# Kernel optimization log

Hardware: AMD Instinct MI355X
Metric: run time of the kernel (lower is better)

## Reference

```python
import jax, jax.numpy as jnp
import numpy as np

V, D, H, L, E = 50000, 128, 128, 4, 160000


def setup_inputs() -> dict:
    key = jax.random.key(0)
    ks = jax.random.split(key, 8)
    inp = {
        "node_embeddings": jax.random.normal(ks[0], (V, D), dtype=jnp.float32),
        "adj0": jax.random.randint(ks[1], (E, 2), 0, V, dtype=jnp.int32),
        "adj1": jax.random.randint(ks[2], (E, 2), 0, V, dtype=jnp.int32),
        "adj2": jax.random.randint(ks[3], (E, 2), 0, V, dtype=jnp.int32),
        "adj3": jax.random.randint(ks[4], (E, 2), 0, V, dtype=jnp.int32),
        # One MLP per (edge_type, endpoint): Linear(2D->H) -> relu -> Linear(H->H), no biases
        "W1": jax.random.normal(ks[5], (L, 2, 2 * D, H), dtype=jnp.float32) * 0.05,
        "W2": jax.random.normal(ks[6], (L, 2, H, H), dtype=jnp.float32) * 0.05,
    }
    return inp


def reference(node_embeddings, adj0, adj1, adj2, adj3, W1, W2):
    num_nodes = node_embeddings.shape[0]
    msgs = []
    tgts = []
    for l, adj in enumerate((adj0, adj1, adj2, adj3)):
        # gather both endpoint states and concat -> [E, 2D]
        src = node_embeddings[adj[:, 0]]
        dst = node_embeddings[adj[:, 1]]
        raw = jnp.concatenate([src, dst], axis=-1)
        # one MLP per endpoint; messages sent to that endpoint's node
        for ep in range(2):
            h = jax.nn.relu(raw @ W1[l, ep])          # [E, H]
            msgs.append(h @ W2[l, ep])                 # [E, H]
            tgts.append(adj[:, ep])
    messages = jnp.concatenate(msgs, axis=0)          # [L*2*E, H]
    targets = jnp.concatenate(tgts, axis=0)           # [L*2*E]
    agg = jax.ops.segment_sum(messages, targets, num_segments=num_nodes)  # [V, H]
    return jax.nn.relu(agg)
```

## Files before the change

### kernel.cpp

```cpp
#include <hip/hip_runtime.h>

#define V_NODES 50000
#define NEDGE   160000
#define NSEG    (8 * V_NODES)

typedef __bf16 bf16;
typedef __attribute__((ext_vector_type(8))) __bf16 bf16x8;
typedef __attribute__((ext_vector_type(4))) __bf16 bf16x4;
typedef __attribute__((ext_vector_type(4))) float  f32x4;

__device__ __forceinline__ int clampV(int n) {
  unsigned u = (unsigned)n;
  return (int)(u < (unsigned)V_NODES ? u : (unsigned)(V_NODES - 1));
}

__device__ __forceinline__ float bflo(unsigned u) {
  return __builtin_bit_cast(float, u << 16);
}
__device__ __forceinline__ float bfhi(unsigned u) {
  return __builtin_bit_cast(float, u & 0xffff0000u);
}


__global__ __launch_bounds__(256) void prep_emb_k(const float* __restrict__ in,
                                                  bf16* __restrict__ out) {
  int i = blockIdx.x * 256 + threadIdx.x;
  float4 v = ((const float4*)in)[i];
  bf16x4 o = {(bf16)v.x, (bf16)v.y, (bf16)v.z, (bf16)v.w};
  *(bf16x4*)(out + (size_t)i * 4) = o;
}

__global__ __launch_bounds__(256) void prep_w1_k(const float* __restrict__ in,
                                                 bf16* __restrict__ out) {
  int idx = blockIdx.x * 256 + threadIdx.x;
  int n = idx & 127, k = (idx >> 7) & 255, g = idx >> 15;
  out[(((g << 7) + n) << 8) + k] = (bf16)in[idx];
}

__global__ __launch_bounds__(256) void prep_w2_k(const float* __restrict__ in,
                                                 bf16* __restrict__ out) {
  int idx = blockIdx.x * 256 + threadIdx.x;
  int n = idx & 127, k = (idx >> 7) & 127, g = idx >> 14;
  out[(((g << 7) + n) << 7) + k] = (bf16)in[idx];
}

__global__ __launch_bounds__(256) void relu_k(float* __restrict__ out) {
  int i = blockIdx.x * 256 + threadIdx.x;
  float4 v = ((float4*)out)[i];
  v.x = fmaxf(v.x, 0.f); v.y = fmaxf(v.y, 0.f);
  v.z = fmaxf(v.z, 0.f); v.w = fmaxf(v.w, 0.f);
  ((float4*)out)[i] = v;
}


__global__ __launch_bounds__(256) void fused_prep_k(
    const float* __restrict__ emb, const float* __restrict__ W1,
    const float* __restrict__ W2,
    const int* __restrict__ a0, const int* __restrict__ a1,
    const int* __restrict__ a2, const int* __restrict__ a3,
    bf16* __restrict__ embB, bf16* __restrict__ w1t, bf16* __restrict__ w2t,
    int* __restrict__ counts) {
  const int bx = blockIdx.x, tid = threadIdx.x;
  if (bx < 6250) {
    int i = bx * 256 + tid;
    float4 v = ((const float4*)emb)[i];
    bf16x4 o = {(bf16)v.x, (bf16)v.y, (bf16)v.z, (bf16)v.w};
    *(bf16x4*)(embB + (size_t)i * 4) = o;
  } else if (bx < 7274) {
    int idx = (bx - 6250) * 256 + tid;
    int n = idx & 127, k = (idx >> 7) & 255, g = idx >> 15;
    w1t[(((g << 7) + n) << 8) + k] = (bf16)W1[idx];
  } else if (bx < 7786) {
    int idx = (bx - 7274) * 256 + tid;
    int n = idx & 127, k = (idx >> 7) & 127, g = idx >> 14;
    w2t[(((g << 7) + n) << 7) + k] = (bf16)W2[idx];
  } else {
    int j = bx - 7786;
    int g = j / 625;
    int e = (j - g * 625) * 256 + tid;
    int l = g >> 1, ep = g & 1;
    const int* adj = (l == 0) ? a0 : (l == 1) ? a1 : (l == 2) ? a2 : a3;
    int tgt = clampV(adj[2 * e + ep]);
    atomicAdd(&counts[g * V_NODES + tgt], 1);
  }
}


__global__ __launch_bounds__(256) void scan_a_k(const int* __restrict__ counts,
                                                int* __restrict__ offs1,
                                                int* __restrict__ bsums) {
  __shared__ int sh[256];
  int t = threadIdx.x, base = blockIdx.x * 512;
  int e0 = base + 2 * t, e1 = e0 + 1;
  int a = (e0 < NSEG) ? counts[e0] : 0;
  int b = (e1 < NSEG) ? counts[e1] : 0;
  int s = a + b;
  sh[t] = s;
  __syncthreads();
  #pragma unroll
  for (int d = 1; d < 256; d <<= 1) {
    int v = (t >= d) ? sh[t - d] : 0;
    __syncthreads();
    sh[t] += v;
    __syncthreads();
  }
  int excl = sh[t] - s;
  if (e0 < NSEG) offs1[e0] = excl;
  if (e1 < NSEG) offs1[e1] = excl + a;
  if (t == 255) bsums[blockIdx.x] = sh[255];
}

#define NBLK_SCAN 782

__global__ __launch_bounds__(256) void scan_b_k(int* __restrict__ bsums,
                                                int* __restrict__ offsX) {
  __shared__ int sh[NBLK_SCAN];
  int t = threadIdx.x;
  for (int i = t; i < NBLK_SCAN; i += 256) sh[i] = bsums[i];
  __syncthreads();
  if (t == 0) {
    int run = 0;
    for (int i = 0; i < NBLK_SCAN; ++i) { int v = sh[i]; sh[i] = run; run += v; }
    offsX[0] = 0;
  }
  __syncthreads();
  for (int i = t; i < NBLK_SCAN; i += 256) bsums[i] = sh[i];
}

__global__ __launch_bounds__(256) void scan_c_k(int* __restrict__ offs1,
                                                const int* __restrict__ bsums) {
  int i = blockIdx.x * 256 + threadIdx.x;
  if (i < NSEG) offs1[i] += bsums[i >> 9];
}


__global__ __launch_bounds__(256) void fused_xg_sc_k(
    const bf16* __restrict__ embB, const bf16* __restrict__ w1t,
    bf16* __restrict__ Xab,
    const int* __restrict__ a0, const int* __restrict__ a1,
    const int* __restrict__ a2, const int* __restrict__ a3,
    int* __restrict__ offs1, int* __restrict__ ids,
    int gbase, int nxg) {
  const int tid = threadIdx.x;
  if ((int)blockIdx.x < nxg) {
    const int slot = blockIdx.x / 625;
    const int bxx  = blockIdx.x - slot * 625;
    const int w = tid >> 6, lane = tid & 63;
    const int l15 = lane & 15, q = lane >> 4;
    const int h2 = w >> 1, dh = w & 1;
    const int g = gbase + slot;

    bf16x8 wA[4][4];
    const bf16* __restrict__ w1g = w1t + (size_t)g * 32768;
    #pragma unroll
    for (int mb = 0; mb < 4; ++mb)
      #pragma unroll
      for (int kb = 0; kb < 4; ++kb)
        wA[mb][kb] = *(const bf16x8*)(w1g + (size_t)(dh * 64 + mb * 16 + l15) * 256 +
                                      h2 * 128 + kb * 32 + q * 8);

    bf16* __restrict__ Xh = Xab + (size_t)slot * 12800000 + (size_t)h2 * 6400000;

    #pragma unroll
    for (int t = 0; t < 5; ++t) {
      const int node = bxx * 80 + t * 16 + l15;
      bf16x8 b[4];
      #pragma unroll
      for (int kb = 0; kb < 4; ++kb)
        b[kb] = *(const bf16x8*)(embB + (size_t)node * 128 + kb * 32 + q * 8);

      f32x4 acc[4] = {};
      #pragma unroll
      for (int kb = 0; kb < 4; ++kb)
        #pragma unroll
        for (int mb = 0; mb < 4; ++mb)
          acc[mb] = __builtin_amdgcn_mfma_f32_16x16x32_bf16(wA[mb][kb], b[kb], acc[mb], 0, 0, 0);

      bf16* basep = Xh + (size_t)node * 128 + dh * 64 + q * 4;
      #pragma unroll
      for (int mb = 0; mb < 4; ++mb) {
        bf16x4 o = {(bf16)acc[mb][0], (bf16)acc[mb][1],
                    (bf16)acc[mb][2], (bf16)acc[mb][3]};
        *(bf16x4*)(basep + mb * 16) = o;
      }
    }
  } else {
    int j = blockIdx.x - nxg;
    int g = j / 625;
    int e = (j - g * 625) * 256 + tid;
    int l = g >> 1, ep = g & 1;
    const int* adj = (l == 0) ? a0 : (l == 1) ? a1 : (l == 2) ? a2 : a3;
    int2 pr = ((const int2*)adj)[e];
    int src = clampV(pr.x), dst = clampV(pr.y);
    int tgt = ep ? dst : src;
    int oth = ep ? src : dst;
    int pos = atomicAdd(&offs1[g * V_NODES + tgt], 1);
    ids[pos] = oth;
  }
}


__global__ __launch_bounds__(256) void aggf4_k(
    const bf16* __restrict__ Xab,
    const int* __restrict__ offsX, const int* __restrict__ ids,
    bf16* __restrict__ HaggB, int gbase) {
  const int wv = threadIdx.x >> 6, lane = threadIdx.x & 63;
  const int h = lane >> 5, m = lane & 31;
  const int node = blockIdx.x * 8 + wv * 2 + h;
  const int slot = blockIdx.y, g = gbase + slot;
  const int ep = g & 1;
  const bf16* __restrict__ Xa = Xab + (size_t)slot * 12800000;
  const bf16* __restrict__ Xb = Xa + 6400000;
  const bf16* __restrict__ own = ep ? Xb : Xa;
  const bf16* __restrict__ oth = ep ? Xa : Xb;
  const int seg = g * V_NODES + node;
  const int beg = offsX[seg], end = offsX[seg + 1];

  uint2 uo = *(const uint2*)(own + (size_t)node * 128 + m * 4);
  const float o0 = bflo(uo.x), o1 = bfhi(uo.x);
  const float o2 = bflo(uo.y), o3 = bfhi(uo.y);

  float s0 = 0.f, s1 = 0.f, s2 = 0.f, s3 = 0.f;
  int i = beg;
  for (; i + 2 <= end; i += 2) {
    int n0 = ids[i];
    int n1 = ids[i + 1];
    uint2 u0 = *(const uint2*)(oth + (size_t)n0 * 128 + m * 4);
    uint2 u1 = *(const uint2*)(oth + (size_t)n1 * 128 + m * 4);
    s0 += fmaxf(o0 + bflo(u0.x), 0.f) + fmaxf(o0 + bflo(u1.x), 0.f);
    s1 += fmaxf(o1 + bfhi(u0.x), 0.f) + fmaxf(o1 + bfhi(u1.x), 0.f);
    s2 += fmaxf(o2 + bflo(u0.y), 0.f) + fmaxf(o2 + bflo(u1.y), 0.f);
    s3 += fmaxf(o3 + bfhi(u0.y), 0.f) + fmaxf(o3 + bfhi(u1.y), 0.f);
  }
  if (i < end) {
    int n = ids[i];
    uint2 u = *(const uint2*)(oth + (size_t)n * 128 + m * 4);
    s0 += fmaxf(o0 + bflo(u.x), 0.f);
    s1 += fmaxf(o1 + bfhi(u.x), 0.f);
    s2 += fmaxf(o2 + bflo(u.y), 0.f);
    s3 += fmaxf(o3 + bfhi(u.y), 0.f);
  }
  bf16x4 st = {(bf16)s0, (bf16)s1, (bf16)s2, (bf16)s3};
  *(bf16x4*)(HaggB + ((size_t)g * V_NODES + node) * 128 + m * 4) = st;
}


__global__ __launch_bounds__(256) void gemm2p_k(const bf16* __restrict__ HaggB,
                                                const bf16* __restrict__ w2t,
                                                float* __restrict__ out) {
  __shared__ __attribute__((aligned(16))) bf16 a_lds[32 * 128];

  const int tid = threadIdx.x, wv = tid >> 6, lane = tid & 63;
  const int l15 = lane & 15, q = lane >> 4;
  const int v0 = blockIdx.x * 32;

  const int srow = tid >> 3, sc0 = (tid & 7) * 2;
  bf16* sp0 = &a_lds[srow * 128 + ((sc0 ^ (srow & 7)) << 3)];
  bf16* sp1 = &a_lds[srow * 128 + (((sc0 + 1) ^ (srow & 7)) << 3)];

  const uint4* Hg = (const uint4*)(HaggB + (size_t)v0 * 128);
  uint4 s0 = Hg[tid * 2], s1 = Hg[tid * 2 + 1];

  f32x4 acc[2][2] = {};
  for (int g = 0; g < 8; ++g) {
    __syncthreads();
    *(uint4*)sp0 = s0;
    *(uint4*)sp1 = s1;
    if (g < 7) {
      const uint4* Hn = (const uint4*)(HaggB + (size_t)(g + 1) * 6400000 +
                                       (size_t)v0 * 128);
      s0 = Hn[tid * 2];
      s1 = Hn[tid * 2 + 1];
    }
    __syncthreads();

    const bf16* __restrict__ Wb = w2t + (size_t)g * 16384;
    #pragma unroll
    for (int kb = 0; kb < 4; ++kb) {
      bf16x8 a[2];
      #pragma unroll
      for (int mt = 0; mt < 2; ++mt) {
        int r = mt * 16 + l15;
        a[mt] = *(const bf16x8*)(&a_lds[r * 128 + (((kb * 4 + q) ^ (r & 7)) << 3)]);
      }
      #pragma unroll
      for (int t = 0; t < 2; ++t) {
        int n = (wv * 2 + t) * 16 + l15;
        bf16x8 b = *(const bf16x8*)(Wb + (size_t)n * 128 + kb * 32 + q * 8);
        #pragma unroll
        for (int mt = 0; mt < 2; ++mt)
          acc[mt][t] = __builtin_amdgcn_mfma_f32_16x16x32_bf16(a[mt], b, acc[mt][t], 0, 0, 0);
      }
    }
  }

  #pragma unroll
  for (int mt = 0; mt < 2; ++mt)
    #pragma unroll
    for (int r = 0; r < 4; ++r) {
      int row = v0 + mt * 16 + q * 4 + r;
      if (row < V_NODES) {
        #pragma unroll
        for (int t = 0; t < 2; ++t) {
          int col = (wv * 2 + t) * 16 + l15;
          out[(size_t)row * 128 + col] = fmaxf(acc[mt][t][r], 0.f);
        }
      }
    }
}


__global__ __launch_bounds__(256) void edge_k(
    const bf16* __restrict__ embB,
    const int* __restrict__ a0, const int* __restrict__ a1,
    const int* __restrict__ a2, const int* __restrict__ a3,
    const bf16* __restrict__ w1t, const bf16* __restrict__ w2t,
    float* __restrict__ out) {

  __shared__ __attribute__((aligned(16))) bf16 w1_lds[128 * 256];
  __shared__ __attribute__((aligned(16))) bf16 h_lds[64 * 128];

  const int tid = threadIdx.x;
  const int g  = blockIdx.x >> 6;
  const int bs = blockIdx.x & 63;
  const int l = g >> 1, ep = g & 1;
  const int* __restrict__ adj = (l == 0) ? a0 : (l == 1) ? a1 : (l == 2) ? a2 : a3;

  {
    const uint4* w1g = (const uint4*)(w1t + (size_t)g * 128 * 256);
    #pragma unroll
    for (int i = 0; i < 16; ++i) {
      int j = i * 256 + tid;
      int n = j >> 5, c = j & 31;
      *(uint4*)(&w1_lds[n * 256 + ((c ^ (n & 7)) << 3)]) = w1g[j];
    }
  }
  __syncthreads();

  const int w    = tid >> 6;
  const int lane = tid & 63;
  const int wr = w >> 1, wc = w & 1;
  const int l15 = lane & 15, q = lane >> 4;
  const bf16* __restrict__ w2g = w2t + (size_t)g * 128 * 128;

  for (int t = bs; t < 2500; t += 64) {
    const int ebase = t * 64;
    int2 pr0 = ((const int2*)adj)[ebase + 32 * wr + l15];
    int2 pr1 = ((const int2*)adj)[ebase + 32 * wr + 16 + l15];
    pr0.x = clampV(pr0.x); pr0.y = clampV(pr0.y);
    pr1.x = clampV(pr1.x); pr1.y = clampV(pr1.y);

    f32x4 acc[2][4] = {};
    #pragma unroll
    for (int kb = 0; kb < 8; ++kb) {
      const int k = kb * 32 + q * 8;
      const int klo = k & 127;
      const int n0 = (kb < 4) ? pr0.x : pr0.y;
      const int n1 = (kb < 4) ? pr1.x : pr1.y;
      bf16x8 a[2], b[4];
      a[0] = *(const bf16x8*)(embB + (size_t)n0 * 128 + klo);
      a[1] = *(const bf16x8*)(embB + (size_t)n1 * 128 + klo);
      const int csw = ((kb << 2) + q);
      #pragma unroll
      for (int nt = 0; nt < 4; ++nt) {
        int n = 64 * wc + 16 * nt + l15;
        b[nt] = *(const bf16x8*)(&w1_lds[n * 256 + ((csw ^ (l15 & 7)) << 3)]);
      }
      #pragma unroll
      for (int mt = 0; mt < 2; ++mt)
        #pragma unroll
        for (int nt = 0; nt < 4; ++nt)
          acc[mt][nt] = __builtin_amdgcn_mfma_f32_16x16x32_bf16(a[mt], b[nt], acc[mt][nt], 0, 0, 0);
    }

    __syncthreads();
    #pragma unroll
    for (int mt = 0; mt < 2; ++mt)
      #pragma unroll
      for (int nt = 0; nt < 4; ++nt)
        #pragma unroll
        for (int r = 0; r < 4; ++r) {
          float v = acc[mt][nt][r];
          v = v > 0.f ? v : 0.f;
          int row = 32 * wr + 16 * mt + 4 * q + r;
          int col = 64 * wc + 16 * nt + l15;
          int c = col >> 3;
          h_lds[row * 128 + (((c ^ (row & 7)) << 3) | (col & 7))] = (bf16)v;
        }
    __syncthreads();

    f32x4 acc2[2][4] = {};
    #pragma unroll
    for (int kb = 0; kb < 4; ++kb) {
      const int k = kb * 32 + q * 8;
      const int csw = (kb << 2) + q;
      bf16x8 a[2], b[4];
      #pragma unroll
      for (int mt = 0; mt < 2; ++mt) {
        int row = 32 * wr + 16 * mt + l15;
        a[mt] = *(const bf16x8*)(&h_lds[row * 128 + ((csw ^ (row & 7)) << 3)]);
      }
      #pragma unroll
      for (int nt = 0; nt < 4; ++nt) {
        int n = 64 * wc + 16 * nt + l15;
        b[nt] = *(const bf16x8*)(w2g + n * 128 + k);
      }
      #pragma unroll
      for (int mt = 0; mt < 2; ++mt)
        #pragma unroll
        for (int nt = 0; nt < 4; ++nt)
          acc2[mt][nt] = __builtin_amdgcn_mfma_f32_16x16x32_bf16(a[mt], b[nt], acc2[mt][nt], 0, 0, 0);
    }

    #pragma unroll
    for (int mt = 0; mt < 2; ++mt)
      #pragma unroll
      for (int r = 0; r < 4; ++r) {
        int row = 32 * wr + 16 * mt + 4 * q + r;
        int2 pr = ((const int2*)adj)[ebase + row];
        int node = clampV(ep ? pr.y : pr.x);
        float* basep = out + (size_t)node * 128 + 64 * wc + l15;
        #pragma unroll
        for (int nt = 0; nt < 4; ++nt)
          unsafeAtomicAdd(basep + 16 * nt, acc2[mt][nt][r]);
      }
  }
}


extern "C" void kernel_launch(void* const* d_in, const int* in_sizes, int n_in,
                              void* d_out, int out_size, void* d_ws, size_t ws_size,
                              hipStream_t stream) {
  const float* emb = (const float*)d_in[0];
  const int* a0 = (const int*)d_in[1];
  const int* a1 = (const int*)d_in[2];
  const int* a2 = (const int*)d_in[3];
  const int* a3 = (const int*)d_in[4];
  const float* W1 = (const float*)d_in[5];
  const float* W2 = (const float*)d_in[6];
  float* out = (float*)d_out;

  char* ws = (char*)d_ws;
  bf16* embB   = (bf16*)(ws);
  bf16* w1t    = (bf16*)(ws + 12800000);
  bf16* w2t    = (bf16*)(ws + 13324288);
  int*  offsX  = (int*) (ws + 13586432);
  int*  ids    = (int*) (ws + 15186448);
  int*  bsums  = (int*) (ws + 20306448);
  int*  counts = (int*) (ws + 20309584);
  bf16* HaggB  = (bf16*)(ws + 21909584);
  bf16* Xab    = (bf16*)(ws + 124309584);
  const size_t fixedsz = 124309584;
  int* offs1 = offsX + 1;

  int GG = 0;
  if      (ws_size >= fixedsz + 8ull * 25600000) GG = 8;
  else if (ws_size >= fixedsz + 4ull * 25600000) GG = 4;
  else if (ws_size >= fixedsz + 2ull * 25600000) GG = 2;
  else if (ws_size >= fixedsz + 1ull * 25600000) GG = 1;

  if (GG) {
    hipMemsetAsync(counts, 0, 1600000, stream);
    fused_prep_k<<<12786, 256, 0, stream>>>(emb, W1, W2, a0, a1, a2, a3,
                                            embB, w1t, w2t, counts);
    scan_a_k<<<NBLK_SCAN, 256, 0, stream>>>(counts, offs1, bsums);
    scan_b_k<<<1, 256, 0, stream>>>(bsums, offsX);
    scan_c_k<<<1563, 256, 0, stream>>>(offs1, bsums);

    fused_xg_sc_k<<<625 * GG + 5000, 256, 0, stream>>>(
        embB, w1t, Xab, a0, a1, a2, a3, offs1, ids, 0, 625 * GG);
    aggf4_k<<<dim3(6250, GG), 256, 0, stream>>>(Xab, offsX, ids, HaggB, 0);

    for (int gb = GG; gb < 8; gb += GG) {
      fused_xg_sc_k<<<625 * GG, 256, 0, stream>>>(
          embB, w1t, Xab, a0, a1, a2, a3, offs1, ids, gb, 625 * GG);
      aggf4_k<<<dim3(6250, GG), 256, 0, stream>>>(Xab, offsX, ids, HaggB, gb);
    }
    gemm2p_k<<<1563, 256, 0, stream>>>(HaggB, w2t, out);
  } else {
    prep_emb_k<<<6250, 256, 0, stream>>>(emb, embB);
    prep_w1_k<<<1024, 256, 0, stream>>>(W1, w1t);
    prep_w2_k<<<512, 256, 0, stream>>>(W2, w2t);
    hipMemsetAsync(d_out, 0, 25600000, stream);
    edge_k<<<512, 256, 0, stream>>>(embB, a0, a1, a2, a3, w1t, w2t, out);
    relu_k<<<6250, 256, 0, stream>>>(out);
  }
}
```

Baseline: 507.2 us.

## Fuse own-side projection, aggregation and second GEMM into one per-node kernel

The first-layer precompute now writes only the 'other endpoint' projection for each group, through an LDS-staged, coalesced store. The own-endpoint projection is recomputed per node inside a new fused kernel. That kernel also does the neighbor gather-relu-sum and the W2 matmul in LDS, accumulating across all 8 groups and applying the final relu. This removes the HaggB intermediate, the half of Xab that held the own side, and the separate gemm2 pass, which cuts global memory traffic and the number of launches. The cost is extra MFMA work for the own projection and serialized per-group barriers inside each block.

```diff
diff --git a/kernel.cpp b/kernel.cpp
--- a/kernel.cpp
+++ b/kernel.cpp
@@ -136,19 +136,20 @@
 
 __global__ __launch_bounds__(256) void fused_xg_sc_k(
     const bf16* __restrict__ embB, const bf16* __restrict__ w1t,
-    bf16* __restrict__ Xab,
+    bf16* __restrict__ Xg,
     const int* __restrict__ a0, const int* __restrict__ a1,
     const int* __restrict__ a2, const int* __restrict__ a3,
-    int* __restrict__ offs1, int* __restrict__ ids,
-    int gbase, int nxg) {
+    int* __restrict__ offs1, int* __restrict__ ids, int nxg) {
+  __shared__ __attribute__((aligned(16))) bf16 stg[2 * 16 * 128];
   const int tid = threadIdx.x;
+
   if ((int)blockIdx.x < nxg) {
-    const int slot = blockIdx.x / 625;
-    const int bxx  = blockIdx.x - slot * 625;
+    const int gp = blockIdx.x / 625, bxx = blockIdx.x - gp * 625;
     const int w = tid >> 6, lane = tid & 63;
     const int l15 = lane & 15, q = lane >> 4;
     const int h2 = w >> 1, dh = w & 1;
-    const int g = gbase + slot;
+    const int g = gp * 2 + h2;
+    const int goff = h2 ? 0 : 128;
 
     bf16x8 wA[4][4];
     const bf16* __restrict__ w1g = w1t + (size_t)g * 32768;
@@ -157,13 +158,15 @@
       #pragma unroll
       for (int kb = 0; kb < 4; ++kb)
         wA[mb][kb] = *(const bf16x8*)(w1g + (size_t)(dh * 64 + mb * 16 + l15) * 256 +
-                                      h2 * 128 + kb * 32 + q * 8);
-
-    bf16* __restrict__ Xh = Xab + (size_t)slot * 12800000 + (size_t)h2 * 6400000;
-
-    #pragma unroll
+                                      goff + kb * 32 + q * 8);
+
+    const int oh = tid >> 7, ln = tid & 127;
+    const int srow = ln >> 3, ch0 = (ln & 7) * 2;
+    const size_t gobase = (size_t)(gp * 2 + oh) * 6400000;
+
     for (int t = 0; t < 5; ++t) {
-      const int node = bxx * 80 + t * 16 + l15;
+      const int nodeB = bxx * 80 + t * 16;
+      const int node = nodeB + l15;
       bf16x8 b[4];
       #pragma unroll
       for (int kb = 0; kb < 4; ++kb)
@@ -176,12 +179,22 @@
         for (int mb = 0; mb < 4; ++mb)
           acc[mb] = __builtin_amdgcn_mfma_f32_16x16x32_bf16(wA[mb][kb], b[kb], acc[mb], 0, 0, 0);
 
-      bf16* basep = Xh + (size_t)node * 128 + dh * 64 + q * 4;
+      if (t) __syncthreads();
       #pragma unroll
       for (int mb = 0; mb < 4; ++mb) {
+        int d0 = dh * 64 + mb * 16 + q * 4;
+        int c = d0 >> 3, sub = (q & 1) * 8;
         bf16x4 o = {(bf16)acc[mb][0], (bf16)acc[mb][1],
                     (bf16)acc[mb][2], (bf16)acc[mb][3]};
-        *(bf16x4*)(basep + mb * 16) = o;
+        *(bf16x4*)((char*)stg + h2 * 4096 + l15 * 256 + ((c ^ (l15 & 7)) << 4) + sub) = o;
+      }
+      __syncthreads();
+      #pragma unroll
+      for (int cc = 0; cc < 2; ++cc) {
+        int ch = ch0 + cc;
+        uint4 v = *(const uint4*)((char*)stg + oh * 4096 + srow * 256 +
+                                  ((ch ^ (srow & 7)) << 4));
+        *(uint4*)(Xg + gobase + (size_t)(nodeB + srow) * 128 + ch * 8) = v;
       }
     }
   } else {
@@ -200,112 +213,112 @@
 }
 
 
-__global__ __launch_bounds__(256) void aggf4_k(
-    const bf16* __restrict__ Xab,
+__global__ __launch_bounds__(256) void agg2_k(
+    const bf16* __restrict__ embB, const bf16* __restrict__ w1t,
+    const bf16* __restrict__ w2t, const bf16* __restrict__ Xg,
     const int* __restrict__ offsX, const int* __restrict__ ids,
-    bf16* __restrict__ HaggB, int gbase) {
-  const int wv = threadIdx.x >> 6, lane = threadIdx.x & 63;
-  const int h = lane >> 5, m = lane & 31;
-  const int node = blockIdx.x * 8 + wv * 2 + h;
-  const int slot = blockIdx.y, g = gbase + slot;
-  const int ep = g & 1;
-  const bf16* __restrict__ Xa = Xab + (size_t)slot * 12800000;
-  const bf16* __restrict__ Xb = Xa + 6400000;
-  const bf16* __restrict__ own = ep ? Xb : Xa;
-  const bf16* __restrict__ oth = ep ? Xa : Xb;
-  const int seg = g * V_NODES + node;
-  const int beg = offsX[seg], end = offsX[seg + 1];
-
-  uint2 uo = *(const uint2*)(own + (size_t)node * 128 + m * 4);
-  const float o0 = bflo(uo.x), o1 = bfhi(uo.x);
-  const float o2 = bflo(uo.y), o3 = bfhi(uo.y);
-
-  float s0 = 0.f, s1 = 0.f, s2 = 0.f, s3 = 0.f;
-  int i = beg;
-  for (; i + 2 <= end; i += 2) {
-    int n0 = ids[i];
-    int n1 = ids[i + 1];
-    uint2 u0 = *(const uint2*)(oth + (size_t)n0 * 128 + m * 4);
-    uint2 u1 = *(const uint2*)(oth + (size_t)n1 * 128 + m * 4);
-    s0 += fmaxf(o0 + bflo(u0.x), 0.f) + fmaxf(o0 + bflo(u1.x), 0.f);
-    s1 += fmaxf(o1 + bfhi(u0.x), 0.f) + fmaxf(o1 + bfhi(u1.x), 0.f);
-    s2 += fmaxf(o2 + bflo(u0.y), 0.f) + fmaxf(o2 + bflo(u1.y), 0.f);
-    s3 += fmaxf(o3 + bfhi(u0.y), 0.f) + fmaxf(o3 + bfhi(u1.y), 0.f);
-  }
-  if (i < end) {
-    int n = ids[i];
-    uint2 u = *(const uint2*)(oth + (size_t)n * 128 + m * 4);
-    s0 += fmaxf(o0 + bflo(u.x), 0.f);
-    s1 += fmaxf(o1 + bfhi(u.x), 0.f);
-    s2 += fmaxf(o2 + bflo(u.y), 0.f);
-    s3 += fmaxf(o3 + bfhi(u.y), 0.f);
-  }
-  bf16x4 st = {(bf16)s0, (bf16)s1, (bf16)s2, (bf16)s3};
-  *(bf16x4*)(HaggB + ((size_t)g * V_NODES + node) * 128 + m * 4) = st;
-}
-
-
-__global__ __launch_bounds__(256) void gemm2p_k(const bf16* __restrict__ HaggB,
-                                                const bf16* __restrict__ w2t,
-                                                float* __restrict__ out) {
-  __shared__ __attribute__((aligned(16))) bf16 a_lds[32 * 128];
+    float* __restrict__ out) {
+  __shared__ __attribute__((aligned(16))) bf16 ownT[16 * 128];
+  __shared__ __attribute__((aligned(16))) bf16 Ht[16 * 128];
 
   const int tid = threadIdx.x, wv = tid >> 6, lane = tid & 63;
   const int l15 = lane & 15, q = lane >> 4;
-  const int v0 = blockIdx.x * 32;
-
-  const int srow = tid >> 3, sc0 = (tid & 7) * 2;
-  bf16* sp0 = &a_lds[srow * 128 + ((sc0 ^ (srow & 7)) << 3)];
-  bf16* sp1 = &a_lds[srow * 128 + (((sc0 + 1) ^ (srow & 7)) << 3)];
-
-  const uint4* Hg = (const uint4*)(HaggB + (size_t)v0 * 128);
-  uint4 s0 = Hg[tid * 2], s1 = Hg[tid * 2 + 1];
-
-  f32x4 acc[2][2] = {};
+  const int v0 = blockIdx.x * 16;
+  const int qw = tid >> 4, j = tid & 15;
+
+  bf16x8 be[4];
+  #pragma unroll
+  for (int kb = 0; kb < 4; ++kb)
+    be[kb] = *(const bf16x8*)(embB + (size_t)(v0 + l15) * 128 + kb * 32 + q * 8);
+
+  f32x4 aco[2] = {};
+
   for (int g = 0; g < 8; ++g) {
-    __syncthreads();
-    *(uint4*)sp0 = s0;
-    *(uint4*)sp1 = s1;
-    if (g < 7) {
-      const uint4* Hn = (const uint4*)(HaggB + (size_t)(g + 1) * 6400000 +
-                                       (size_t)v0 * 128);
-      s0 = Hn[tid * 2];
-      s1 = Hn[tid * 2 + 1];
-    }
-    __syncthreads();
-
-    const bf16* __restrict__ Wb = w2t + (size_t)g * 16384;
+    const int ownoff = (g & 1) ? 128 : 0;
+    const bf16* __restrict__ w1g = w1t + (size_t)g * 32768;
+
+    f32x4 oc[2] = {};
+    #pragma unroll
+    for (int kb = 0; kb < 4; ++kb)
+      #pragma unroll
+      for (int t = 0; t < 2; ++t) {
+        int m = (wv * 2 + t) * 16 + l15;
+        bf16x8 a = *(const bf16x8*)(w1g + (size_t)m * 256 + ownoff + kb * 32 + q * 8);
+        oc[t] = __builtin_amdgcn_mfma_f32_16x16x32_bf16(a, be[kb], oc[t], 0, 0, 0);
+      }
+    #pragma unroll
+    for (int t = 0; t < 2; ++t) {
+      int d0 = (wv * 2 + t) * 16 + q * 4;
+      int c = d0 >> 3, sub = (q & 1) * 8;
+      bf16x4 o = {(bf16)oc[t][0], (bf16)oc[t][1], (bf16)oc[t][2], (bf16)oc[t][3]};
+      *(bf16x4*)((char*)ownT + l15 * 256 + ((c ^ (l15 & 7)) << 4) + sub) = o;
+    }
+    __syncthreads();
+
+    {
+      const int nd = qw;
+      const int seg = g * V_NODES + v0 + nd;
+      const int beg = offsX[seg], end = offsX[seg + 1];
+      uint4 uo = *(const uint4*)((char*)ownT + nd * 256 + ((j ^ (nd & 7)) << 4));
+      const float o0 = bflo(uo.x), o1 = bfhi(uo.x), o2 = bflo(uo.y), o3 = bfhi(uo.y);
+      const float o4 = bflo(uo.z), o5 = bfhi(uo.z), o6 = bflo(uo.w), o7 = bfhi(uo.w);
+      const bf16* __restrict__ Xgg = Xg + (size_t)g * 6400000;
+
+      float s0 = 0.f, s1 = 0.f, s2 = 0.f, s3 = 0.f;
+      float s4 = 0.f, s5 = 0.f, s6 = 0.f, s7 = 0.f;
+      int i = beg;
+      for (; i + 2 <= end; i += 2) {
+        int n0 = ids[i], n1 = ids[i + 1];
+        uint4 u0 = *(const uint4*)(Xgg + (size_t)n0 * 128 + j * 8);
+        uint4 u1 = *(const uint4*)(Xgg + (size_t)n1 * 128 + j * 8);
+        s0 += fmaxf(o0 + bflo(u0.x), 0.f) + fmaxf(o0 + bflo(u1.x), 0.f);
+        s1 += fmaxf(o1 + bfhi(u0.x), 0.f) + fmaxf(o1 + bfhi(u1.x), 0.f);
+        s2 += fmaxf(o2 + bflo(u0.y), 0.f) + fmaxf(o2 + bflo(u1.y), 0.f);
+        s3 += fmaxf(o3 + bfhi(u0.y), 0.f) + fmaxf(o3 + bfhi(u1.y), 0.f);
+        s4 += fmaxf(o4 + bflo(u0.z), 0.f) + fmaxf(o4 + bflo(u1.z), 0.f);
+        s5 += fmaxf(o5 + bfhi(u0.z), 0.f) + fmaxf(o5 + bfhi(u1.z), 0.f);
+        s6 += fmaxf(o6 + bflo(u0.w), 0.f) + fmaxf(o6 + bflo(u1.w), 0.f);
+        s7 += fmaxf(o7 + bfhi(u0.w), 0.f) + fmaxf(o7 + bfhi(u1.w), 0.f);
+      }
+      if (i < end) {
+        int n = ids[i];
+        uint4 u = *(const uint4*)(Xgg + (size_t)n * 128 + j * 8);
+        s0 += fmaxf(o0 + bflo(u.x), 0.f);
+        s1 += fmaxf(o1 + bfhi(u.x), 0.f);
+        s2 += fmaxf(o2 + bflo(u.y), 0.f);
+        s3 += fmaxf(o3 + bfhi(u.y), 0.f);
+        s4 += fmaxf(o4 + bflo(u.z), 0.f);
+        s5 += fmaxf(o5 + bfhi(u.z), 0.f);
+        s6 += fmaxf(o6 + bflo(u.w), 0.f);
+        s7 += fmaxf(o7 + bfhi(u.w), 0.f);
+      }
+      bf16x8 hv = {(bf16)s0, (bf16)s1, (bf16)s2, (bf16)s3,
+                   (bf16)s4, (bf16)s5, (bf16)s6, (bf16)s7};
+      *(bf16x8*)((char*)Ht + nd * 256 + ((j ^ (nd & 7)) << 4)) = hv;
+    }
+    __syncthreads();
+
+    const bf16* __restrict__ w2g = w2t + (size_t)g * 16384;
     #pragma unroll
     for (int kb = 0; kb < 4; ++kb) {
-      bf16x8 a[2];
-      #pragma unroll
-      for (int mt = 0; mt < 2; ++mt) {
-        int r = mt * 16 + l15;
-        a[mt] = *(const bf16x8*)(&a_lds[r * 128 + (((kb * 4 + q) ^ (r & 7)) << 3)]);
-      }
+      int c2 = kb * 4 + q;
+      bf16x8 a2 = *(const bf16x8*)((char*)Ht + l15 * 256 + ((c2 ^ (l15 & 7)) << 4));
       #pragma unroll
       for (int t = 0; t < 2; ++t) {
         int n = (wv * 2 + t) * 16 + l15;
-        bf16x8 b = *(const bf16x8*)(Wb + (size_t)n * 128 + kb * 32 + q * 8);
-        #pragma unroll
-        for (int mt = 0; mt < 2; ++mt)
-          acc[mt][t] = __builtin_amdgcn_mfma_f32_16x16x32_bf16(a[mt], b, acc[mt][t], 0, 0, 0);
+        bf16x8 b2 = *(const bf16x8*)(w2g + (size_t)n * 128 + kb * 32 + q * 8);
+        aco[t] = __builtin_amdgcn_mfma_f32_16x16x32_bf16(a2, b2, aco[t], 0, 0, 0);
       }
     }
   }
 
   #pragma unroll
-  for (int mt = 0; mt < 2; ++mt)
+  for (int t = 0; t < 2; ++t)
     #pragma unroll
     for (int r = 0; r < 4; ++r) {
-      int row = v0 + mt * 16 + q * 4 + r;
-      if (row < V_NODES) {
-        #pragma unroll
-        for (int t = 0; t < 2; ++t) {
-          int col = (wv * 2 + t) * 16 + l15;
-          out[(size_t)row * 128 + col] = fmaxf(acc[mt][t][r], 0.f);
-        }
-      }
+      int row = v0 + q * 4 + r;
+      int col = (wv * 2 + t) * 16 + l15;
+      out[(size_t)row * 128 + col] = fmaxf(aco[t][r], 0.f);
     }
 }
 
@@ -448,18 +461,11 @@
   int*  ids    = (int*) (ws + 15186448);
   int*  bsums  = (int*) (ws + 20306448);
   int*  counts = (int*) (ws + 20309584);
-  bf16* HaggB  = (bf16*)(ws + 21909584);
-  bf16* Xab    = (bf16*)(ws + 124309584);
-  const size_t fixedsz = 124309584;
+  bf16* Xg     = (bf16*)(ws + 21909584);
+  const size_t need = 124309584;
   int* offs1 = offsX + 1;
 
-  int GG = 0;
-  if      (ws_size >= fixedsz + 8ull * 25600000) GG = 8;
-  else if (ws_size >= fixedsz + 4ull * 25600000) GG = 4;
-  else if (ws_size >= fixedsz + 2ull * 25600000) GG = 2;
-  else if (ws_size >= fixedsz + 1ull * 25600000) GG = 1;
-
-  if (GG) {
+  if (ws_size >= need) {
     hipMemsetAsync(counts, 0, 1600000, stream);
     fused_prep_k<<<12786, 256, 0, stream>>>(emb, W1, W2, a0, a1, a2, a3,
                                             embB, w1t, w2t, counts);
@@ -467,16 +473,9 @@
     scan_b_k<<<1, 256, 0, stream>>>(bsums, offsX);
     scan_c_k<<<1563, 256, 0, stream>>>(offs1, bsums);
 
-    fused_xg_sc_k<<<625 * GG + 5000, 256, 0, stream>>>(
-        embB, w1t, Xab, a0, a1, a2, a3, offs1, ids, 0, 625 * GG);
-    aggf4_k<<<dim3(6250, GG), 256, 0, stream>>>(Xab, offsX, ids, HaggB, 0);
-
-    for (int gb = GG; gb < 8; gb += GG) {
-      fused_xg_sc_k<<<625 * GG, 256, 0, stream>>>(
-          embB, w1t, Xab, a0, a1, a2, a3, offs1, ids, gb, 625 * GG);
-      aggf4_k<<<dim3(6250, GG), 256, 0, stream>>>(Xab, offsX, ids, HaggB, gb);
-    }
-    gemm2p_k<<<1563, 256, 0, stream>>>(HaggB, w2t, out);
+    fused_xg_sc_k<<<7500, 256, 0, stream>>>(embB, w1t, Xg, a0, a1, a2, a3,
+                                            offs1, ids, 2500);
+    agg2_k<<<3125, 256, 0, stream>>>(embB, w1t, w2t, Xg, offsX, ids, out);
   } else {
     prep_emb_k<<<6250, 256, 0, stream>>>(emb, embB);
     prep_w1_k<<<1024, 256, 0, stream>>>(W1, w1t);
```

Result: slower. 554.8 us (+9.4%).

## Stage X-projection output through swizzled LDS for coalesced stores, fix 4-group batching

Applied to the files above, without the earlier changes.

The MFMA results of the per-node W1 projection are written to a shared-memory tile using an XOR swizzle, then read back so each thread issues full 16-byte row-contiguous global stores. Previously each lane wrote scattered 8-byte fragments. The aim is to improve write coalescing of the large Xab intermediate. It also removes the adaptive group-count logic and always processes groups in two batches of four, which requires a fixed workspace size and adds two block barriers per tile.

```diff
diff --git a/kernel.cpp b/kernel.cpp
--- a/kernel.cpp
+++ b/kernel.cpp
@@ -134,17 +134,18 @@
 }
 
 
-__global__ __launch_bounds__(256) void fused_xg_sc_k(
+__global__ __launch_bounds__(256) void fused_xab_sc_k(
     const bf16* __restrict__ embB, const bf16* __restrict__ w1t,
     bf16* __restrict__ Xab,
     const int* __restrict__ a0, const int* __restrict__ a1,
     const int* __restrict__ a2, const int* __restrict__ a3,
     int* __restrict__ offs1, int* __restrict__ ids,
     int gbase, int nxg) {
+  __shared__ __attribute__((aligned(16))) bf16 stg[2 * 16 * 128];
   const int tid = threadIdx.x;
+
   if ((int)blockIdx.x < nxg) {
-    const int slot = blockIdx.x / 625;
-    const int bxx  = blockIdx.x - slot * 625;
+    const int slot = blockIdx.x / 625, bxx = blockIdx.x - slot * 625;
     const int w = tid >> 6, lane = tid & 63;
     const int l15 = lane & 15, q = lane >> 4;
     const int h2 = w >> 1, dh = w & 1;
@@ -159,11 +160,13 @@
         wA[mb][kb] = *(const bf16x8*)(w1g + (size_t)(dh * 64 + mb * 16 + l15) * 256 +
                                       h2 * 128 + kb * 32 + q * 8);
 
-    bf16* __restrict__ Xh = Xab + (size_t)slot * 12800000 + (size_t)h2 * 6400000;
-
-    #pragma unroll
+    const int oh = tid >> 7, ln = tid & 127;
+    const int srow = ln >> 3, ch0 = (ln & 7) * 2;
+    bf16* __restrict__ Xout = Xab + (size_t)slot * 12800000 + (size_t)oh * 6400000;
+
     for (int t = 0; t < 5; ++t) {
-      const int node = bxx * 80 + t * 16 + l15;
+      const int nodeB = bxx * 80 + t * 16;
+      const int node = nodeB + l15;
       bf16x8 b[4];
       #pragma unroll
       for (int kb = 0; kb < 4; ++kb)
@@ -176,12 +179,22 @@
         for (int mb = 0; mb < 4; ++mb)
           acc[mb] = __builtin_amdgcn_mfma_f32_16x16x32_bf16(wA[mb][kb], b[kb], acc[mb], 0, 0, 0);
 
-      bf16* basep = Xh + (size_t)node * 128 + dh * 64 + q * 4;
+      if (t) __syncthreads();
       #pragma unroll
       for (int mb = 0; mb < 4; ++mb) {
+        int d0 = dh * 64 + mb * 16 + q * 4;
+        int c = d0 >> 3, sub = (q & 1) * 8;
         bf16x4 o = {(bf16)acc[mb][0], (bf16)acc[mb][1],
                     (bf16)acc[mb][2], (bf16)acc[mb][3]};
-        *(bf16x4*)(basep + mb * 16) = o;
+        *(bf16x4*)((char*)stg + h2 * 4096 + l15 * 256 + ((c ^ (l15 & 7)) << 4) + sub) = o;
+      }
+      __syncthreads();
+      #pragma unroll
+      for (int cc = 0; cc < 2; ++cc) {
+        int ch = ch0 + cc;
+        uint4 v = *(const uint4*)((char*)stg + oh * 4096 + srow * 256 +
+                                  ((ch ^ (srow & 7)) << 4));
+        *(uint4*)(Xout + (size_t)(nodeB + srow) * 128 + ch * 8) = v;
       }
     }
   } else {
@@ -450,16 +463,10 @@
   int*  counts = (int*) (ws + 20309584);
   bf16* HaggB  = (bf16*)(ws + 21909584);
   bf16* Xab    = (bf16*)(ws + 124309584);
-  const size_t fixedsz = 124309584;
+  const size_t need = 226709584;
   int* offs1 = offsX + 1;
 
-  int GG = 0;
-  if      (ws_size >= fixedsz + 8ull * 25600000) GG = 8;
-  else if (ws_size >= fixedsz + 4ull * 25600000) GG = 4;
-  else if (ws_size >= fixedsz + 2ull * 25600000) GG = 2;
-  else if (ws_size >= fixedsz + 1ull * 25600000) GG = 1;
-
-  if (GG) {
+  if (ws_size >= need) {
     hipMemsetAsync(counts, 0, 1600000, stream);
     fused_prep_k<<<12786, 256, 0, stream>>>(emb, W1, W2, a0, a1, a2, a3,
                                             embB, w1t, w2t, counts);
@@ -467,15 +474,14 @@
     scan_b_k<<<1, 256, 0, stream>>>(bsums, offsX);
     scan_c_k<<<1563, 256, 0, stream>>>(offs1, bsums);
 
-    fused_xg_sc_k<<<625 * GG + 5000, 256, 0, stream>>>(
-        embB, w1t, Xab, a0, a1, a2, a3, offs1, ids, 0, 625 * GG);
-    aggf4_k<<<dim3(6250, GG), 256, 0, stream>>>(Xab, offsX, ids, HaggB, 0);
-
-    for (int gb = GG; gb < 8; gb += GG) {
-      fused_xg_sc_k<<<625 * GG, 256, 0, stream>>>(
-          embB, w1t, Xab, a0, a1, a2, a3, offs1, ids, gb, 625 * GG);
-      aggf4_k<<<dim3(6250, GG), 256, 0, stream>>>(Xab, offsX, ids, HaggB, gb);
-    }
+    fused_xab_sc_k<<<7500, 256, 0, stream>>>(embB, w1t, Xab, a0, a1, a2, a3,
+                                             offs1, ids, 0, 2500);
+    aggf4_k<<<dim3(6250, 4), 256, 0, stream>>>(Xab, offsX, ids, HaggB, 0);
+
+    fused_xab_sc_k<<<2500, 256, 0, stream>>>(embB, w1t, Xab, a0, a1, a2, a3,
+                                             offs1, ids, 4, 2500);
+    aggf4_k<<<dim3(6250, 4), 256, 0, stream>>>(Xab, offsX, ids, HaggB, 4);
+
     gemm2p_k<<<1563, 256, 0, stream>>>(HaggB, w2t, out);
   } else {
     prep_emb_k<<<6250, 256, 0, stream>>>(emb, embB);
```

Result: faster. 496.4 us (-2.1%).
